# Optimization experiments

Measured on AMD Instinct MI355X. Metric: run time of the kernel, lower is better.

## Reference

```python
import jax, jax.numpy as jnp
import numpy as np

NEG = -1e30  # finite stand-in for -inf in the sparse-softmax mask


def setup_inputs() -> dict:
    key = jax.random.key(0)
    kh, kwl, kwn, kn = jax.random.split(key, 4)
    B, S, D, E = 8, 4096, 1024, 64
    return {
        "h": jax.random.normal(kh, (B, S, D), dtype=jnp.float32),
        "Wl": jax.random.normal(kwl, (E, D), dtype=jnp.float32) * 0.02,
        "bl": jnp.zeros((E,), dtype=jnp.float32),
        "Wn": jax.random.normal(kwn, (E, D), dtype=jnp.float32) * 0.02,
        "bn": jnp.zeros((E,), dtype=jnp.float32),
        "noise": jax.random.normal(kn, (B, S, E), dtype=jnp.float32),
        "top_k": 2,
    }


def reference(h, Wl, bl, Wn, bn, noise, top_k):
    # logits, noise std: two small linears over the expert dim
    logits = jnp.einsum("bsd,ed->bse", h, Wl) + bl          # [B,S,E]
    std = jax.nn.softplus(jnp.einsum("bsd,ed->bse", h, Wn) + bn)
    noisy = logits + noise * std                              # [B,S,E]

    full_p = jax.nn.softmax(noisy, axis=-1)

    topk_vals, ix = jax.lax.top_k(noisy, top_k)               # [B,S,k]
    E = noisy.shape[-1]
    # scatter top-k values back into a -inf-filled tensor == mask non-topk
    mask = jax.nn.one_hot(ix, E, dtype=jnp.bool_).any(axis=-2)  # [B,S,E]
    sparse = jnp.where(mask, noisy, NEG)
    route_p = jax.nn.softmax(sparse, axis=-1)
    return route_p, ix, full_p
```

## Files before the change

### kernel.cpp

```cpp
#include <hip/hip_runtime.h>
#include <math.h>


#define DIM 1024
#define NEXP 64
#define LS 40
#define CS 132
#define LOSCALE 2048.0f
#define INV_LOSCALE (1.0f / 2048.0f)

using half4v   = __attribute__((ext_vector_type(4)))  _Float16;
using half8v   = __attribute__((ext_vector_type(8)))  _Float16;
using floatx16 = __attribute__((ext_vector_type(16))) float;

__device__ inline void split4(const float4 v, half4v& hi, half4v& lo) {
    _Float16 h0 = (_Float16)v.x, h1 = (_Float16)v.y,
             h2 = (_Float16)v.z, h3 = (_Float16)v.w;
    hi = (half4v){h0, h1, h2, h3};
    lo = (half4v){(_Float16)((v.x - (float)h0) * LOSCALE),
                  (_Float16)((v.y - (float)h1) * LOSCALE),
                  (_Float16)((v.z - (float)h2) * LOSCALE),
                  (_Float16)((v.w - (float)h3) * LOSCALE)};
}

__device__ inline half8v mk8(const half4v a, const half4v b) {
    return (half8v){a[0], a[1], a[2], a[3], b[0], b[1], b[2], b[3]};
}

#define MFMA32(a, b, c) __builtin_amdgcn_mfma_f32_32x32x16_f16((a), (b), (c), 0, 0, 0)

__global__ __launch_bounds__(64)
void split_B(const float* __restrict__ Wl, const float* __restrict__ Wn,
             _Float16* __restrict__ bhi, _Float16* __restrict__ blo)
{
    const int g = blockIdx.x * 64 + threadIdx.x;
    const int lane = g & 63;
    const int f    = (g >> 6) & 63;
    const int nc   = g >> 12;
    const int e = nc * 32 + (lane & 31);
    const int k = f * 16 + (lane >> 5) * 8;
    const float* W = ((e < NEXP) ? (Wl + (size_t)e * DIM)
                                 : (Wn + (size_t)(e - NEXP) * DIM)) + k;
    float4 v0 = *(const float4*)(W);
    float4 v1 = *(const float4*)(W + 4);
    half4v h0, l0, h1, l1;
    split4(v0, h0, l0);
    split4(v1, h1, l1);
    *(half8v*)(bhi + (size_t)g * 8) = mk8(h0, h1);
    *(half8v*)(blo + (size_t)g * 8) = mk8(l0, l1);
}

__global__ __launch_bounds__(128, 2)
void router_main(const float* __restrict__ h, const _Float16* __restrict__ bhi,
                 const _Float16* __restrict__ blo, const float* __restrict__ bl,
                 const float* __restrict__ bn, const float* __restrict__ noise,
                 float* __restrict__ outR, float* __restrict__ outIx,
                 float* __restrict__ outF, int M)
{
    __shared__ float smem[2 * 32 * CS];

    const int tid   = threadIdx.x;
    const int wv    = tid >> 6;
    const int lane  = tid & 63;
    const int row31 = lane & 31;
    const int oct   = lane >> 5;
    const int tok0  = blockIdx.x * 32;
    const int kbase = wv * 512;

    _Float16* Abase = (_Float16*)smem + wv * 5120;

    const int arow = lane >> 1, acol = lane & 1;
    const float* hp = h + (size_t)(tok0 + arow) * DIM + kbase + acol * 16;
    const int sA = arow * LS + acol * 16;
    const int fA = row31 * LS + oct * 8;

    const _Float16* bhp = bhi + (size_t)lane * 8 + (size_t)(wv * 16) * 2 * 512;
    const _Float16* blp = blo + (size_t)lane * 8 + (size_t)(wv * 16) * 2 * 512;

    floatx16 acc1[4], acc2[4];
#pragma unroll
    for (int nc = 0; nc < 4; nc++)
#pragma unroll
        for (int i = 0; i < 16; i++) { acc1[nc][i] = 0.f; acc2[nc][i] = 0.f; }

    float4 av[4];
#pragma unroll
    for (int q = 0; q < 4; q++) av[q] = *(const float4*)(hp + q * 4);

    for (int t = 0; t < 16; t++) {
        _Float16* Ahi = Abase + (t & 1) * 2560;
        _Float16* Alo = Ahi + 1280;
#pragma unroll
        for (int q = 0; q < 4; q++) {
            half4v hi, lo;
            split4(av[q], hi, lo);
            *(half4v*)(Ahi + sA + q * 4) = hi;
            *(half4v*)(Alo + sA + q * 4) = lo;
        }
        half8v aH[2], aL[2];
#pragma unroll
        for (int ks = 0; ks < 2; ks++) {
            aH[ks] = *(const half8v*)(Ahi + fA + ks * 16);
            aL[ks] = *(const half8v*)(Alo + fA + ks * 16);
        }
        if (t < 15) {
#pragma unroll
            for (int q = 0; q < 4; q++)
                av[q] = *(const float4*)(hp + (t + 1) * 32 + q * 4);
        }
#pragma unroll
        for (int nc = 0; nc < 4; nc++) {
#pragma unroll
            for (int ks = 0; ks < 2; ks++) {
                const size_t off = (size_t)(nc * 64 + t * 2 + ks) * 512;
                half8v bH = *(const half8v*)(bhp + off);
                half8v bL = *(const half8v*)(blp + off);
                acc1[nc] = MFMA32(aH[ks], bH, acc1[nc]);
                acc2[nc] = MFMA32(aH[ks], bL, acc2[nc]);
                acc2[nc] = MFMA32(aL[ks], bH, acc2[nc]);
            }
        }
    }

    __syncthreads();

    float* Cs = smem + wv * (32 * CS);
#pragma unroll
    for (int nc = 0; nc < 4; nc++) {
#pragma unroll
        for (int i = 0; i < 16; i++) {
            int rowt = (i & 3) + 8 * (i >> 2) + 4 * oct;
            Cs[rowt * CS + nc * 32 + row31] = acc1[nc][i] + acc2[nc][i] * INV_LOSCALE;
        }
    }
    __syncthreads();

    const float blv = bl[lane];
    const float bnv = bn[lane];
    const float* Cs0 = smem;
    const float* Cs1 = smem + 32 * CS;

    for (int i = 0; i < 16; i++) {
        const int t = wv * 16 + i;
        const int gt = tok0 + t;
        float xr = Cs0[t * CS + lane] + Cs1[t * CS + lane] + blv;
        float xf = Cs0[t * CS + 64 + lane] + Cs1[t * CS + 64 + lane] + bnv;
        float nz = noise[(size_t)gt * NEXP + lane];

        float stdv = fmaxf(xf, 0.f) + log1pf(expf(-fabsf(xf)));
        float noisy = fmaf(nz, stdv, xr);

        float m = noisy;
#pragma unroll
        for (int o = 32; o > 0; o >>= 1) m = fmaxf(m, __shfl_xor(m, o, 64));
        float p = expf(noisy - m);
        float s = p;
#pragma unroll
        for (int o = 32; o > 0; o >>= 1) s += __shfl_xor(s, o, 64);
        float fullp = p / s;

        float v = noisy; int idx = lane;
#pragma unroll
        for (int o = 32; o > 0; o >>= 1) {
            float ov = __shfl_xor(v, o, 64);
            int   oi = __shfl_xor(idx, o, 64);
            if (ov > v || (ov == v && oi < idx)) { v = ov; idx = oi; }
        }
        const float v1 = v; const int i1 = idx;
        v = (lane == i1) ? -INFINITY : noisy; idx = lane;
#pragma unroll
        for (int o = 32; o > 0; o >>= 1) {
            float ov = __shfl_xor(v, o, 64);
            int   oi = __shfl_xor(idx, o, 64);
            if (ov > v || (ov == v && oi < idx)) { v = ov; idx = oi; }
        }
        const float v2 = v; const int i2 = idx;

        float e2 = expf(v2 - v1);
        float den = 1.f + e2;
        float routep = (lane == i1) ? (1.f / den) : ((lane == i2) ? (e2 / den) : 0.f);

        outR[(size_t)gt * NEXP + lane] = routep;
        outF[(size_t)gt * NEXP + lane] = fullp;
        if (lane == 0) {
            outIx[(size_t)gt * 2 + 0] = (float)i1;
            outIx[(size_t)gt * 2 + 1] = (float)i2;
        }
    }
}

extern "C" void kernel_launch(void* const* d_in, const int* in_sizes, int n_in,
                              void* d_out, int out_size, void* d_ws, size_t ws_size,
                              hipStream_t stream) {
    const float* h     = (const float*)d_in[0];
    const float* Wl    = (const float*)d_in[1];
    const float* bl    = (const float*)d_in[2];
    const float* Wn    = (const float*)d_in[3];
    const float* bn    = (const float*)d_in[4];
    const float* noise = (const float*)d_in[5];
    float* out = (float*)d_out;

    const int M = in_sizes[0] / DIM;
    float* outR  = out;
    float* outIx = out + (size_t)M * NEXP;
    float* outF  = outIx + (size_t)M * 2;

    _Float16* bhi = (_Float16*)d_ws;
    _Float16* blo = bhi + 128 * DIM;

    split_B<<<256, 64, 0, stream>>>(Wl, Wn, bhi, blo);
    router_main<<<M / 32, 128, 0, stream>>>(h, bhi, blo, bl, bn, noise,
                                            outR, outIx, outF, M);
}
```

Before: 259.5 us.

## Split expert columns across four waves and load A directly to registers

Changes the work split so each of four waves owns one 32-column chunk of the 128 outputs over the full K range, instead of two waves splitting K with all four chunks each. The A tile is now loaded straight from global memory into MFMA operand registers and split into fp16 hi/lo per wave, dropping the LDS staging and the cross-wave K reduction. This cuts accumulator registers and raises occupancy, at the cost of each wave re-reading and re-splitting the same h rows, which means four times the h loads per block.

```diff
diff --git a/kernel.cpp b/kernel.cpp
--- a/kernel.cpp
+++ b/kernel.cpp
@@ -4,7 +4,6 @@
 
 #define DIM 1024
 #define NEXP 64
-#define LS 40
 #define CS 132
 #define LOSCALE 2048.0f
 #define INV_LOSCALE (1.0f / 2048.0f)
@@ -35,10 +34,10 @@
 {
     const int g = blockIdx.x * 64 + threadIdx.x;
     const int lane = g & 63;
-    const int f    = (g >> 6) & 63;
+    const int t    = (g >> 6) & 63;
     const int nc   = g >> 12;
     const int e = nc * 32 + (lane & 31);
-    const int k = f * 16 + (lane >> 5) * 8;
+    const int k = t * 16 + (lane >> 5) * 8;
     const float* W = ((e < NEXP) ? (Wl + (size_t)e * DIM)
                                  : (Wn + (size_t)(e - NEXP) * DIM)) + k;
     float4 v0 = *(const float4*)(W);
@@ -50,14 +49,14 @@
     *(half8v*)(blo + (size_t)g * 8) = mk8(l0, l1);
 }
 
-__global__ __launch_bounds__(128, 2)
+__global__ __launch_bounds__(256, 4)
 void router_main(const float* __restrict__ h, const _Float16* __restrict__ bhi,
                  const _Float16* __restrict__ blo, const float* __restrict__ bl,
                  const float* __restrict__ bn, const float* __restrict__ noise,
                  float* __restrict__ outR, float* __restrict__ outIx,
                  float* __restrict__ outF, int M)
 {
-    __shared__ float smem[2 * 32 * CS];
+    __shared__ float Cs[32 * CS];
 
     const int tid   = threadIdx.x;
     const int wv    = tid >> 6;
@@ -65,86 +64,54 @@
     const int row31 = lane & 31;
     const int oct   = lane >> 5;
     const int tok0  = blockIdx.x * 32;
-    const int kbase = wv * 512;
 
-    _Float16* Abase = (_Float16*)smem + wv * 5120;
+    const float* hp = h + (size_t)(tok0 + row31) * DIM + oct * 8;
+    const _Float16* bbh = bhi + (size_t)(wv * 64) * 512 + lane * 8;
+    const _Float16* bbl = blo + (size_t)(wv * 64) * 512 + lane * 8;
 
-    const int arow = lane >> 1, acol = lane & 1;
-    const float* hp = h + (size_t)(tok0 + arow) * DIM + kbase + acol * 16;
-    const int sA = arow * LS + acol * 16;
-    const int fA = row31 * LS + oct * 8;
+    floatx16 acc1, acc2;
+#pragma unroll
+    for (int i = 0; i < 16; i++) { acc1[i] = 0.f; acc2[i] = 0.f; }
 
-    const _Float16* bhp = bhi + (size_t)lane * 8 + (size_t)(wv * 16) * 2 * 512;
-    const _Float16* blp = blo + (size_t)lane * 8 + (size_t)(wv * 16) * 2 * 512;
+    float4 a0c = *(const float4*)(hp);
+    float4 a1c = *(const float4*)(hp + 4);
+    half8v bhc = *(const half8v*)(bbh);
+    half8v blc = *(const half8v*)(bbl);
 
-    floatx16 acc1[4], acc2[4];
-#pragma unroll
-    for (int nc = 0; nc < 4; nc++)
-#pragma unroll
-        for (int i = 0; i < 16; i++) { acc1[nc][i] = 0.f; acc2[nc][i] = 0.f; }
-
-    float4 av[4];
-#pragma unroll
-    for (int q = 0; q < 4; q++) av[q] = *(const float4*)(hp + q * 4);
-
-    for (int t = 0; t < 16; t++) {
-        _Float16* Ahi = Abase + (t & 1) * 2560;
-        _Float16* Alo = Ahi + 1280;
-#pragma unroll
-        for (int q = 0; q < 4; q++) {
-            half4v hi, lo;
-            split4(av[q], hi, lo);
-            *(half4v*)(Ahi + sA + q * 4) = hi;
-            *(half4v*)(Alo + sA + q * 4) = lo;
+#pragma unroll 4
+    for (int t = 0; t < 64; t++) {
+        float4 a0n, a1n; half8v bhn, bln;
+        if (t + 1 < 64) {
+            a0n = *(const float4*)(hp + (t + 1) * 16);
+            a1n = *(const float4*)(hp + (t + 1) * 16 + 4);
+            bhn = *(const half8v*)(bbh + (t + 1) * 512);
+            bln = *(const half8v*)(bbl + (t + 1) * 512);
         }
-        half8v aH[2], aL[2];
-#pragma unroll
-        for (int ks = 0; ks < 2; ks++) {
-            aH[ks] = *(const half8v*)(Ahi + fA + ks * 16);
-            aL[ks] = *(const half8v*)(Alo + fA + ks * 16);
-        }
-        if (t < 15) {
-#pragma unroll
-            for (int q = 0; q < 4; q++)
-                av[q] = *(const float4*)(hp + (t + 1) * 32 + q * 4);
-        }
-#pragma unroll
-        for (int nc = 0; nc < 4; nc++) {
-#pragma unroll
-            for (int ks = 0; ks < 2; ks++) {
-                const size_t off = (size_t)(nc * 64 + t * 2 + ks) * 512;
-                half8v bH = *(const half8v*)(bhp + off);
-                half8v bL = *(const half8v*)(blp + off);
-                acc1[nc] = MFMA32(aH[ks], bH, acc1[nc]);
-                acc2[nc] = MFMA32(aH[ks], bL, acc2[nc]);
-                acc2[nc] = MFMA32(aL[ks], bH, acc2[nc]);
-            }
-        }
+        half4v h0, l0, h1, l1;
+        split4(a0c, h0, l0);
+        split4(a1c, h1, l1);
+        half8v aH = mk8(h0, h1), aL = mk8(l0, l1);
+        acc1 = MFMA32(aH, bhc, acc1);
+        acc2 = MFMA32(aH, blc, acc2);
+        acc2 = MFMA32(aL, bhc, acc2);
+        a0c = a0n; a1c = a1n; bhc = bhn; blc = bln;
     }
 
-    __syncthreads();
-
-    float* Cs = smem + wv * (32 * CS);
 #pragma unroll
-    for (int nc = 0; nc < 4; nc++) {
-#pragma unroll
-        for (int i = 0; i < 16; i++) {
-            int rowt = (i & 3) + 8 * (i >> 2) + 4 * oct;
-            Cs[rowt * CS + nc * 32 + row31] = acc1[nc][i] + acc2[nc][i] * INV_LOSCALE;
-        }
+    for (int i = 0; i < 16; i++) {
+        int rowt = (i & 3) + 8 * (i >> 2) + 4 * oct;
+        Cs[rowt * CS + wv * 32 + row31] = acc1[i] + acc2[i] * INV_LOSCALE;
     }
     __syncthreads();
 
     const float blv = bl[lane];
     const float bnv = bn[lane];
-    const float* Cs0 = smem;
-    const float* Cs1 = smem + 32 * CS;
 
-    for (int i = 0; i < 16; i++) {
-        const int t = wv * 16 + i;
+    for (int i = 0; i < 8; i++) {
+        const int t = wv * 8 + i;
         const int gt = tok0 + t;
-        float xr = Cs0[t * CS + lane] + Cs1[t * CS + lane] + blv;
-        float xf = Cs0[t * CS + 64 + lane] + Cs1[t * CS + 64 + lane] + bnv;
+        float xr = Cs[t * CS + lane] + blv;
+        float xf = Cs[t * CS + 64 + lane] + bnv;
         float nz = noise[(size_t)gt * NEXP + lane];
 
         float stdv = fmaxf(xf, 0.f) + log1pf(expf(-fabsf(xf)));
@@ -209,6 +176,6 @@
     _Float16* blo = bhi + 128 * DIM;
 
     split_B<<<256, 64, 0, stream>>>(Wl, Wn, bhi, blo);
-    router_main<<<M / 32, 128, 0, stream>>>(h, bhi, blo, bl, bn, noise,
+    router_main<<<M / 32, 256, 0, stream>>>(h, bhi, blo, bl, bn, noise,
                                             outR, outIx, outF, M);
 }
```

New measurement: 280.2 us. 8.0% more time.
